# Performance work log

Measured on AMD Instinct MI355X. Metric: run time of the kernel, lower is better.

Reference implementation:

```python
import jax, jax.numpy as jnp
import numpy as np

N_CROPS = 64
K = 128          # keypoints per crop (uniform ragged special case)
D = 128          # descriptor dim
KNN = 20
NQ = 20
MIN_V, MAX_V = 0.0, 1.0


def setup_inputs() -> dict:
    key = jax.random.key(0)
    k1, k2 = jax.random.split(key)
    b = N_CROPS * K
    anc = jax.random.normal(k1, (b, D), dtype=jnp.float32)
    pos = jax.random.normal(k2, (b, D), dtype=jnp.float32)
    # L2-normalized descriptors so similarities fall in the quantizer range
    anc = anc / jnp.linalg.norm(anc, axis=1, keepdims=True)
    pos = pos / jnp.linalg.norm(pos, axis=1, keepdims=True)
    kpts_crop_ids = np.full((N_CROPS,), K, dtype=np.int32)
    return {"anc_feat": anc, "pos_feat": pos, "kpts_crop_ids": kpts_crop_ids}


def _neg_cols(n_crops, k, b):
    # Static per-crop column indices into sim_neg_all (width b-1), excluding
    # the same-crop negative block [i*k, i*k + (k-1)) exactly as the torch code.
    all_c = np.arange(b - 1)
    cols = []
    for i in range(n_crops):
        c = i * k
        cols.append(np.concatenate([all_c[:c], all_c[c + k - 1:]]))
    return np.stack(cols)  # [n_crops, b-k]


def compute_ap(x, label, nq=NQ, min_v=MIN_V, max_v=MAX_V):
    # R2D2 APLoss.compute_AP: fixed 1x1-conv quantizer -> triangular bins
    a = (nq - 1) / (max_v - min_v)
    w1 = np.full(nq, -a, np.float32)
    b1 = (a * min_v + np.arange(nq, 0, -1)).astype(np.float32)
    w2 = np.full(nq, a, np.float32)
    b2 = (np.arange(2 - nq, 2) - a * min_v).astype(np.float32)
    w1[0], b1[0] = 0.0, 1.0     # first line of 1st half: horizontal
    w2[-1], b2[-1] = 0.0, 1.0   # last line of 2nd half: horizontal
    xq = x[:, None, :]
    q = jnp.minimum(w1[None, :, None] * xq + b1[None, :, None],
                    w2[None, :, None] * xq + b2[None, :, None])
    q = jnp.clip(q, 0.0)                                 # N x Q x M
    nbs = q.sum(-1)                                      # N x Q
    rec = (q * label[:, None, :]).sum(-1)                # N x Q
    prec = jnp.cumsum(rec, -1) / (1e-16 + jnp.cumsum(nbs, -1))
    rec = rec / rec.sum(-1, keepdims=True)
    return (prec * rec).sum(-1)                          # per-query AP, [N]


def reference(anc_feat, pos_feat, kpts_crop_ids):
    ks = np.asarray(kpts_crop_ids)
    assert np.all(ks == ks[0]) and int(ks[0]) > 1, "uniform crops, >1 kpt each"
    k = int(ks[0]); n_crops = ks.shape[0]; b = n_crops * k
    sim = anc_feat @ pos_feat.T                          # [b, b]
    sim_pos = jnp.diagonal(sim)[:, None]                 # [b, 1]
    # drop diagonal -> [b, b-1] (row-major off-diagonal, same as mtx[~eye])
    sim_neg_all = sim.reshape(-1)[:-1].reshape(b - 1, b + 1)[:, 1:].reshape(b, b - 1)
    cols = jnp.asarray(_neg_cols(n_crops, k, b))         # [n_crops, b-k]
    blocks = sim_neg_all.reshape(n_crops, k, b - 1)
    # exclude same-crop negatives per crop (static gather), then hard-neg top-k
    excl = jnp.take_along_axis(blocks, cols[:, None, :], axis=2)  # [n_crops, k, b-k]
    top, _ = jax.lax.top_k(excl, KNN)                    # sorted descending == sort[:, :knn]
    sim_neg = top.reshape(b, KNN)
    sim_final = jnp.concatenate([sim_pos, sim_neg], axis=1)      # [b, knn+1]
    lbl_final = jnp.zeros_like(sim_final).at[:, 0].set(1.0)
    ap = compute_ap(sim_final, lbl_final)
    return (1.0 - ap).mean(), ap.mean()
```

## Files before the change

kernel.cpp:

```cpp
#include <hip/hip_runtime.h>

#define B_TOT 8192
#define DIM 128
#define KNN 20
#define NQ 20

#define RPB 128
#define SLICE 1024
#define NSLICE 8
#define NSTEP 16
#define NBIN 64
#define CBUF 64
#define CSTRIDE 66

typedef float f32x4 __attribute__((ext_vector_type(4)));
typedef short short8 __attribute__((ext_vector_type(8)));

__device__ __forceinline__ unsigned short f2bf(float f) {
  unsigned u = __float_as_uint(f);
  return (unsigned short)((u + 0x7FFFu + ((u >> 16) & 1u)) >> 16);
}
__device__ __forceinline__ float bf2f(unsigned short u) {
  return __uint_as_float(((unsigned)u) << 16);
}
__device__ __forceinline__ int binof(float v) {
  int b = (int)((v + 1.0f) * 32.0f);
  return min(NBIN - 1, max(0, b));
}

__global__ __launch_bounds__(256) void cvt_bf16(
    const float* __restrict__ a, const float* __restrict__ p,
    unsigned short* __restrict__ ab, unsigned short* __restrict__ pb) {
  const int i = (blockIdx.x * 256 + threadIdx.x) * 4;
  const float4 va = *reinterpret_cast<const float4*>(a + i);
  const float4 vp = *reinterpret_cast<const float4*>(p + i);
  ushort4 ra, rp;
  ra.x = f2bf(va.x); ra.y = f2bf(va.y); ra.z = f2bf(va.z); ra.w = f2bf(va.w);
  rp.x = f2bf(vp.x); rp.y = f2bf(vp.y); rp.z = f2bf(vp.z); rp.w = f2bf(vp.w);
  *reinterpret_cast<ushort4*>(ab + i) = ra;
  *reinterpret_cast<ushort4*>(pb + i) = rp;
}

__global__ __launch_bounds__(512) void apk_slice(
    const unsigned short* __restrict__ ancb,
    const unsigned short* __restrict__ posb,
    unsigned short* __restrict__ gTop,
    float* __restrict__ gDiag)
{
  __shared__ unsigned int sHist[RPB][NBIN];
  __shared__ unsigned short sBuf[RPB][CSTRIDE];
  __shared__ int sCnt[RPB];
  __shared__ int sThrB[RPB];

  const int tid = threadIdx.x;
  const int wave = tid >> 6;
  const int lane = tid & 63;
  const int rt = wave >> 1;
  const int cg = wave & 1;
  const int l15 = lane & 15;
  const int g = lane >> 4;
  const int rg = blockIdx.x >> 3;
  const int cs = blockIdx.x & 7;
  const int rBase = rg * RPB;
  const int sx0 = (cs == (rg >> 3)) ? (rg & 7) * 2 : -9;

  for (int i = tid; i < RPB * NBIN; i += 512) (&sHist[0][0])[i] = 0u;
  for (int i = tid; i < RPB; i += 512) sCnt[i] = 0;

  short8 afr[2][4];
#pragma unroll
  for (int rsub = 0; rsub < 2; ++rsub) {
    const short8* arow = reinterpret_cast<const short8*>(
        ancb + (size_t)(rBase + rt * 32 + rsub * 16 + l15) * DIM);
#pragma unroll
    for (int kk = 0; kk < 4; ++kk) afr[rsub][kk] = arow[kk * 4 + g];
  }
  __syncthreads();

#define LOADB_MFMA(S)                                                         \
  const int c0 = cs * SLICE + (S) * 64 + cg * 32 + l15;                       \
  short8 bfr[2][4];                                                           \
  _Pragma("unroll") for (int csub = 0; csub < 2; ++csub) {                    \
    const unsigned short* bp = posb + (size_t)(c0 + csub * 16) * DIM + g * 8; \
    _Pragma("unroll") for (int kk = 0; kk < 4; ++kk)                          \
      bfr[csub][kk] = *reinterpret_cast<const short8*>(bp + kk * 32);         \
  }                                                                           \
  f32x4 acc[2][2];                                                            \
  _Pragma("unroll") for (int rsub = 0; rsub < 2; ++rsub)                      \
  _Pragma("unroll") for (int csub = 0; csub < 2; ++csub) {                    \
    acc[rsub][csub] = 0.f;                                                    \
    _Pragma("unroll") for (int kk = 0; kk < 4; ++kk)                          \
      acc[rsub][csub] = __builtin_amdgcn_mfma_f32_16x16x32_bf16(              \
          afr[rsub][kk], bfr[csub][kk], acc[rsub][csub], 0, 0, 0);            \
  }

#pragma unroll 2
  for (int s = 0; s < NSTEP; ++s) {
    LOADB_MFMA(s)
    if (s == sx0 || s == sx0 + 1) {
      const int soff = s - sx0;
#pragma unroll
      for (int rsub = 0; rsub < 2; ++rsub)
#pragma unroll
        for (int csub = 0; csub < 2; ++csub)
#pragma unroll
          for (int q = 0; q < 4; ++q) {
            const int row_l = rt * 32 + rsub * 16 + g * 4 + q;
            const int col_l = cg * 32 + csub * 16 + l15;
            if (row_l == soff * 64 + col_l)
              gDiag[rBase + row_l] = acc[rsub][csub][q];
          }
    } else {
#pragma unroll
      for (int rsub = 0; rsub < 2; ++rsub)
#pragma unroll
        for (int q = 0; q < 4; ++q) {
          const int row_l = rt * 32 + rsub * 16 + g * 4 + q;
          atomicAdd(&sHist[row_l][binof(acc[rsub][0][q])], 1u);
          atomicAdd(&sHist[row_l][binof(acc[rsub][1][q])], 1u);
        }
    }
  }
  __syncthreads();

  if (tid < RPB) {
    int cum = 0, bstar = 0;
    for (int b = NBIN - 1; b >= 0; --b) {
      cum += (int)sHist[tid][b];
      if (cum >= KNN) { bstar = b; break; }
    }
    sThrB[tid] = bstar;
  }
  __syncthreads();

  int thrb[2][4];
#pragma unroll
  for (int rsub = 0; rsub < 2; ++rsub)
#pragma unroll
    for (int q = 0; q < 4; ++q)
      thrb[rsub][q] = sThrB[rt * 32 + rsub * 16 + g * 4 + q];

#pragma unroll 2
  for (int s = 0; s < NSTEP; ++s) {
    if (s == sx0 || s == sx0 + 1) continue;
    LOADB_MFMA(s)
#pragma unroll
    for (int rsub = 0; rsub < 2; ++rsub)
#pragma unroll
      for (int q = 0; q < 4; ++q) {
        const int row_l = rt * 32 + rsub * 16 + g * 4 + q;
        const float v0 = acc[rsub][0][q];
        const float v1 = acc[rsub][1][q];
        if (binof(v0) >= thrb[rsub][q]) {
          const int idx = atomicAdd(&sCnt[row_l], 1);
          if (idx < CBUF) sBuf[row_l][idx] = f2bf(v0);
        }
        if (binof(v1) >= thrb[rsub][q]) {
          const int idx = atomicAdd(&sCnt[row_l], 1);
          if (idx < CBUF) sBuf[row_l][idx] = f2bf(v1);
        }
      }
  }
  __syncthreads();

  const int row = tid >> 2;
  const int h = tid & 3;
  const int cnt = min(sCnt[row], CBUF);
  float tk[KNN];
#pragma unroll
  for (int q = 0; q < KNN; ++q) tk[q] = -1e30f;
  for (int i = h; i < cnt; i += 4) {
    const float v = bf2f(sBuf[row][i]);
    if (v > tk[0]) {
      float x = v;
#pragma unroll
      for (int p = 0; p < KNN - 1; ++p) {
        const float nxt = tk[p + 1];
        tk[p] = fminf(x, nxt);
        x = fmaxf(x, nxt);
      }
      tk[KNN - 1] = x;
    }
  }
  unsigned short* mrg = reinterpret_cast<unsigned short*>(&sHist[row][0]);
#pragma unroll
  for (int q = 0; q < KNN; ++q) mrg[h * KNN + q] = f2bf(tk[q]);
  if (h < 2) {
    float out[KNN];
    int a = KNN - 1, b = KNN - 1;
#pragma unroll
    for (int o = KNN - 1; o >= 0; --o) {
      const float va = (a >= 0) ? bf2f(mrg[h * KNN + a]) : -3e30f;
      const float vb = (b >= 0) ? bf2f(mrg[(h + 2) * KNN + b]) : -3e30f;
      if (va >= vb) { out[o] = va; --a; } else { out[o] = vb; --b; }
    }
#pragma unroll
    for (int q = 0; q < KNN; ++q) mrg[h * KNN + q] = f2bf(out[q]);
  }
  if (h == 0) {
    float out[KNN];
    int a = KNN - 1, b = KNN - 1;
#pragma unroll
    for (int o = KNN - 1; o >= 0; --o) {
      const float va = (a >= 0) ? bf2f(mrg[a]) : -3e30f;
      const float vb = (b >= 0) ? bf2f(mrg[KNN + b]) : -3e30f;
      if (va >= vb) { out[o] = va; --a; } else { out[o] = vb; --b; }
    }
#pragma unroll
    for (int q = 0; q < KNN; ++q)
      gTop[(size_t)(rBase + row) * (NSLICE * KNN) + cs * KNN + q] = f2bf(out[q]);
  }
}

__global__ __launch_bounds__(256) void apk_reduce(
    const unsigned short* __restrict__ gTop, const float* __restrict__ gDiag,
    float* __restrict__ apsum)
{
  const int row = blockIdx.x * 256 + threadIdx.x;
  float tk[KNN];
#pragma unroll
  for (int q = 0; q < KNN; ++q) tk[q] = -1e30f;
  const unsigned short* tp = gTop + (size_t)row * (NSLICE * KNN);
  for (int i = 0; i < NSLICE * KNN; ++i) {
    const float v = bf2f(tp[i]);
    if (v > tk[0]) {
      float x = v;
#pragma unroll
      for (int p = 0; p < KNN - 1; ++p) {
        const float nxt = tk[p + 1];
        tk[p] = fminf(x, nxt);
        x = fmaxf(x, nxt);
      }
      tk[KNN - 1] = x;
    }
  }
  float x[KNN + 1];
  x[0] = gDiag[row];
#pragma unroll
  for (int q = 0; q < KNN; ++q) x[q + 1] = tk[q];
  float cum_rec = 0.f, cum_nbs = 0.f, ap_num = 0.f;
#pragma unroll 1
  for (int qi = 0; qi < NQ; ++qi) {
    const float w1 = (qi == 0) ? 0.f : -19.f;
    const float c1 = (qi == 0) ? 1.f : (float)(20 - qi);
    const float w2 = (qi == NQ - 1) ? 0.f : 19.f;
    const float c2 = (qi == NQ - 1) ? 1.f : (float)(qi - 18);
    float nbs = 0.f, rec = 0.f;
#pragma unroll
    for (int jx = 0; jx < KNN + 1; ++jx) {
      const float xv = x[jx];
      float qv = fminf(fmaf(w1, xv, c1), fmaf(w2, xv, c2));
      qv = fmaxf(qv, 0.f);
      nbs += qv;
      if (jx == 0) rec = qv;
    }
    cum_rec += rec;
    cum_nbs += nbs;
    ap_num = fmaf(cum_rec / (1e-16f + cum_nbs), rec, ap_num);
  }
  float ap = ap_num / cum_rec;
#pragma unroll
  for (int o = 1; o < 64; o <<= 1) ap += __shfl_xor(ap, o, 64);
  if ((threadIdx.x & 63) == 0) atomicAdd(apsum, ap);
}

#define F_TM 16
#define F_TN 256
#define F_NTILE (B_TOT / F_TN)
#define F_TPR (F_TN / F_TM)
#define F_SSTRIDE 264
#define KCROP 128

__global__ __launch_bounds__(256) void apk_topk_f32(
    const float* __restrict__ anc, const float* __restrict__ pos,
    float* __restrict__ apsum)
{
  __shared__ __align__(16) float sAnc[F_TM][DIM];
  __shared__ float sSim[F_TM * F_SSTRIDE];
  __shared__ float sTop[F_TM][F_TPR][KNN];
  __shared__ float sDiag[F_TM];
  __shared__ float sAp[F_TM];
  const int tid = threadIdx.x;
  const int rowBase = blockIdx.x * F_TM;
  for (int idx = tid; idx < F_TM * DIM; idx += 256)
    sAnc[idx / DIM][idx % DIM] = anc[rowBase * DIM + idx];
  __syncthreads();
  float tk[KNN];
#pragma unroll
  for (int q = 0; q < KNN; ++q) tk[q] = -1e30f;
  const int cropLo = (rowBase >> 7) << 7;
  const int myRow = tid / F_TPR;
  const int myLane = tid % F_TPR;
  for (int t = 0; t < F_NTILE; ++t) {
    const int j = t * F_TN + tid;
    float acc[F_TM];
#pragma unroll
    for (int r = 0; r < F_TM; ++r) acc[r] = 0.f;
    const float4* pj = reinterpret_cast<const float4*>(pos + (size_t)j * DIM);
#pragma unroll 2
    for (int k4 = 0; k4 < DIM / 4; ++k4) {
      const float4 p = pj[k4];
#pragma unroll
      for (int r = 0; r < F_TM; ++r) {
        const float4 a = *reinterpret_cast<const float4*>(&sAnc[r][k4 * 4]);
        acc[r] = fmaf(p.x, a.x, acc[r]);
        acc[r] = fmaf(p.y, a.y, acc[r]);
        acc[r] = fmaf(p.z, a.z, acc[r]);
        acc[r] = fmaf(p.w, a.w, acc[r]);
      }
    }
    if (j >= rowBase && j < rowBase + F_TM) sDiag[j - rowBase] = acc[j - rowBase];
    __syncthreads();
#pragma unroll
    for (int r = 0; r < F_TM; ++r) sSim[r * F_SSTRIDE + tid] = acc[r];
    __syncthreads();
    const int jbase = t * F_TN;
#pragma unroll
    for (int q = 0; q < F_TN / F_TPR; ++q) {
      const int jj = q * F_TPR + myLane;
      const int jg = jbase + jj;
      const float v = sSim[myRow * F_SSTRIDE + jj];
      if ((unsigned)(jg - cropLo) >= (unsigned)KCROP && v > tk[0]) {
        float x = v;
#pragma unroll
        for (int p = 0; p < KNN - 1; ++p) {
          const float nxt = tk[p + 1];
          tk[p] = fminf(x, nxt);
          x = fmaxf(x, nxt);
        }
        tk[KNN - 1] = x;
      }
    }
  }
  __syncthreads();
#pragma unroll
  for (int q = 0; q < KNN; ++q) sTop[myRow][myLane][q] = tk[q];
  __syncthreads();
  for (int step = F_TPR / 2; step > 0; step >>= 1) {
    if (myLane < step) {
      float out[KNN];
      int a = KNN - 1, b = KNN - 1;
#pragma unroll
      for (int o = KNN - 1; o >= 0; --o) {
        const float va = (a >= 0) ? sTop[myRow][myLane][a] : -3e30f;
        const float vb = (b >= 0) ? sTop[myRow][myLane + step][b] : -3e30f;
        if (va >= vb) { out[o] = va; --a; } else { out[o] = vb; --b; }
      }
#pragma unroll
      for (int q = 0; q < KNN; ++q) sTop[myRow][myLane][q] = out[q];
    }
    __syncthreads();
  }
  if (tid < F_TM) {
    float x[KNN + 1];
    x[0] = sDiag[tid];
#pragma unroll
    for (int q = 0; q < KNN; ++q) x[q + 1] = sTop[tid][0][q];
    float cum_rec = 0.f, cum_nbs = 0.f, ap_num = 0.f;
#pragma unroll 1
    for (int qi = 0; qi < NQ; ++qi) {
      const float w1 = (qi == 0) ? 0.f : -19.f;
      const float c1 = (qi == 0) ? 1.f : (float)(20 - qi);
      const float w2 = (qi == NQ - 1) ? 0.f : 19.f;
      const float c2 = (qi == NQ - 1) ? 1.f : (float)(qi - 18);
      float nbs = 0.f, rec = 0.f;
#pragma unroll
      for (int jx = 0; jx < KNN + 1; ++jx) {
        const float xv = x[jx];
        float qv = fminf(fmaf(w1, xv, c1), fmaf(w2, xv, c2));
        qv = fmaxf(qv, 0.f);
        nbs += qv;
        if (jx == 0) rec = qv;
      }
      cum_rec += rec;
      cum_nbs += nbs;
      ap_num = fmaf(cum_rec / (1e-16f + cum_nbs), rec, ap_num);
    }
    sAp[tid] = ap_num / cum_rec;
  }
  __syncthreads();
  if (tid == 0) {
    float s = 0.f;
#pragma unroll
    for (int r = 0; r < F_TM; ++r) s += sAp[r];
    atomicAdd(apsum, s);
  }
}

__global__ void apk_final(const float* __restrict__ apsum, float* __restrict__ out) {
  const float m = *apsum * (1.f / (float)B_TOT);
  out[0] = 1.f - m;
  out[1] = m;
}

extern "C" void kernel_launch(void* const* d_in, const int* in_sizes, int n_in,
                              void* d_out, int out_size, void* d_ws, size_t ws_size,
                              hipStream_t stream) {
  const float* anc = (const float*)d_in[0];
  const float* pos = (const float*)d_in[1];
  const size_t bf_bytes = (size_t)B_TOT * DIM * sizeof(unsigned short);
  const size_t top_bytes = (size_t)B_TOT * NSLICE * KNN * sizeof(unsigned short);
  const size_t diag_bytes = (size_t)B_TOT * sizeof(float);
  const size_t off_top = 2 * bf_bytes;
  const size_t off_diag = off_top + ((top_bytes + 15) & ~(size_t)15);
  const size_t off_sum = off_diag + ((diag_bytes + 15) & ~(size_t)15);
  const size_t need = off_sum + 16;
  if (ws_size >= need) {
    unsigned short* ancb = (unsigned short*)d_ws;
    unsigned short* posb = ancb + (size_t)B_TOT * DIM;
    unsigned short* gTop = (unsigned short*)((char*)d_ws + off_top);
    float* gDiag = (float*)((char*)d_ws + off_diag);
    float* apsum = (float*)((char*)d_ws + off_sum);
    hipMemsetAsync(apsum, 0, sizeof(float), stream);
    cvt_bf16<<<(B_TOT * DIM) / (256 * 4), 256, 0, stream>>>(anc, pos, ancb, posb);
    apk_slice<<<64 * NSLICE, 512, 0, stream>>>(ancb, posb, gTop, gDiag);
    apk_reduce<<<B_TOT / 256, 256, 0, stream>>>(gTop, gDiag, apsum);
    apk_final<<<1, 1, 0, stream>>>(apsum, (float*)d_out);
  } else {
    float* apsum = (float*)d_ws;
    hipMemsetAsync(apsum, 0, sizeof(float), stream);
    apk_topk_f32<<<B_TOT / F_TM, 256, 0, stream>>>(anc, pos, apsum);
    apk_final<<<1, 1, 0, stream>>>(apsum, (float*)d_out);
  }
}
```

Before: 246.5 us.

## Replace histogram pass with sampled threshold and fuse reduce/final via last-block atomics

Drops the two-pass histogram approach, in which every tile was computed twice. Instead, a top-20 threshold is estimated per row from a 256-column sample, and candidates above it are collected in a single pass over the remaining tiles. The separate reduce kernel, final kernel and memset are folded into apk_slice: counters are zeroed in cvt_bf16, and the last-arriving block per row group does the cross-slice merge and the AP computation, while the last row group writes the output. This removes one full MFMA recompute and three launches. In exchange it adds serialized top-k work on the sample and threadfence/atomic completion logic, and the candidate buffer can overflow if the sampled threshold is loose.

```diff
diff --git a/kernel.cpp b/kernel.cpp
--- a/kernel.cpp
+++ b/kernel.cpp
@@ -9,9 +9,7 @@
 #define SLICE 1024
 #define NSLICE 8
 #define NSTEP 16
-#define NBIN 64
-#define CBUF 64
-#define CSTRIDE 66
+#define USTRIDE 264
 
 typedef float f32x4 __attribute__((ext_vector_type(4)));
 typedef short short8 __attribute__((ext_vector_type(8)));
@@ -23,14 +21,12 @@
 __device__ __forceinline__ float bf2f(unsigned short u) {
   return __uint_as_float(((unsigned)u) << 16);
 }
-__device__ __forceinline__ int binof(float v) {
-  int b = (int)((v + 1.0f) * 32.0f);
-  return min(NBIN - 1, max(0, b));
-}
 
 __global__ __launch_bounds__(256) void cvt_bf16(
     const float* __restrict__ a, const float* __restrict__ p,
-    unsigned short* __restrict__ ab, unsigned short* __restrict__ pb) {
+    unsigned short* __restrict__ ab, unsigned short* __restrict__ pb,
+    unsigned int* __restrict__ ctrs) {
+  if (blockIdx.x == 0 && threadIdx.x < 66) ctrs[threadIdx.x] = 0u;
   const int i = (blockIdx.x * 256 + threadIdx.x) * 4;
   const float4 va = *reinterpret_cast<const float4*>(a + i);
   const float4 vp = *reinterpret_cast<const float4*>(p + i);
@@ -41,16 +37,44 @@
   *reinterpret_cast<ushort4*>(pb + i) = rp;
 }
 
+#define BUBBLE(tk, v)                                                         \
+  if ((v) > (tk)[0]) {                                                        \
+    float x_ = (v);                                                           \
+    _Pragma("unroll") for (int p_ = 0; p_ < KNN - 1; ++p_) {                  \
+      const float nxt_ = (tk)[p_ + 1];                                        \
+      (tk)[p_] = fminf(x_, nxt_);                                             \
+      x_ = fmaxf(x_, nxt_);                                                   \
+    }                                                                         \
+    (tk)[KNN - 1] = x_;                                                       \
+  }
+
+#define MERGE2(mrg, o1, o2, out)                                              \
+  {                                                                           \
+    int a_ = KNN - 1, b_ = KNN - 1;                                           \
+    _Pragma("unroll") for (int o_ = KNN - 1; o_ >= 0; --o_) {                 \
+      const float va_ = (a_ >= 0) ? bf2f((mrg)[(o1) * KNN + a_]) : -3e30f;    \
+      const float vb_ = (b_ >= 0) ? bf2f((mrg)[(o2) * KNN + b_]) : -3e30f;    \
+      if (va_ >= vb_) { (out)[o_] = va_; --a_; } else { (out)[o_] = vb_; --b_; } \
+    }                                                                         \
+  }
+
 __global__ __launch_bounds__(512) void apk_slice(
     const unsigned short* __restrict__ ancb,
     const unsigned short* __restrict__ posb,
     unsigned short* __restrict__ gTop,
-    float* __restrict__ gDiag)
+    float* __restrict__ gDiag,
+    unsigned int* __restrict__ ctrs,
+    float* __restrict__ outp)
 {
-  __shared__ unsigned int sHist[RPB][NBIN];
-  __shared__ unsigned short sBuf[RPB][CSTRIDE];
+  __shared__ unsigned short sU[RPB][USTRIDE];
   __shared__ int sCnt[RPB];
-  __shared__ int sThrB[RPB];
+  __shared__ float sThr[RPB];
+  __shared__ float sAp[RPB];
+  __shared__ int sIsLast;
+
+  float* apsum = reinterpret_cast<float*>(ctrs);
+  unsigned int* rgDone = ctrs + 1;
+  unsigned int* gReady = ctrs + 2;
 
   const int tid = threadIdx.x;
   const int wave = tid >> 6;
@@ -63,9 +87,7 @@
   const int cs = blockIdx.x & 7;
   const int rBase = rg * RPB;
   const int sx0 = (cs == (rg >> 3)) ? (rg & 7) * 2 : -9;
-
-  for (int i = tid; i < RPB * NBIN; i += 512) (&sHist[0][0])[i] = 0u;
-  for (int i = tid; i < RPB; i += 512) sCnt[i] = 0;
+  const int sampBase = (sx0 >= 0 && sx0 < 4) ? 4 : 0;
 
   short8 afr[2][4];
 #pragma unroll
@@ -75,7 +97,6 @@
 #pragma unroll
     for (int kk = 0; kk < 4; ++kk) afr[rsub][kk] = arow[kk * 4 + g];
   }
-  __syncthreads();
 
 #define LOADB_MFMA(S)                                                         \
   const int c0 = cs * SLICE + (S) * 64 + cg * 32 + l15;                       \
@@ -94,8 +115,60 @@
           afr[rsub][kk], bfr[csub][kk], acc[rsub][csub], 0, 0, 0);            \
   }
 
-#pragma unroll 2
+  for (int s = sampBase; s < sampBase + 4; ++s) {
+    LOADB_MFMA(s)
+#pragma unroll
+    for (int rsub = 0; rsub < 2; ++rsub)
+#pragma unroll
+      for (int csub = 0; csub < 2; ++csub)
+#pragma unroll
+        for (int q = 0; q < 4; ++q) {
+          const int row_l = rt * 32 + rsub * 16 + g * 4 + q;
+          const int sc = (s - sampBase) * 64 + cg * 32 + csub * 16 + l15;
+          sU[row_l][sc] = f2bf(acc[rsub][csub][q]);
+        }
+  }
+  __syncthreads();
+
+  {
+    const int row = tid >> 2;
+    const int h = tid & 3;
+    float tk[KNN];
+#pragma unroll
+    for (int q = 0; q < KNN; ++q) tk[q] = -1e30f;
+    for (int i = 0; i < 64; ++i) {
+      const float v = bf2f(sU[row][h + i * 4]);
+      BUBBLE(tk, v)
+    }
+    unsigned short* mrg = &sU[row][0];
+#pragma unroll
+    for (int q = 0; q < KNN; ++q) mrg[h * KNN + q] = f2bf(tk[q]);
+    if (h < 2) {
+      float out[KNN];
+      MERGE2(mrg, h, h + 2, out)
+#pragma unroll
+      for (int q = 0; q < KNN; ++q) mrg[h * KNN + q] = f2bf(out[q]);
+    }
+    if (h == 0) {
+      float out[KNN];
+      MERGE2(mrg, 0, 1, out)
+#pragma unroll
+      for (int q = 0; q < KNN; ++q) mrg[q] = f2bf(out[q]);
+      sCnt[row] = KNN;
+      sThr[row] = out[0];
+    }
+  }
+  __syncthreads();
+
+  float thrv[2][4];
+#pragma unroll
+  for (int rsub = 0; rsub < 2; ++rsub)
+#pragma unroll
+    for (int q = 0; q < 4; ++q)
+      thrv[rsub][q] = sThr[rt * 32 + rsub * 16 + g * 4 + q];
+
   for (int s = 0; s < NSTEP; ++s) {
+    if ((unsigned)(s - sampBase) < 4u) continue;
     LOADB_MFMA(s)
     if (s == sx0 || s == sx0 + 1) {
       const int soff = s - sx0;
@@ -116,152 +189,134 @@
 #pragma unroll
         for (int q = 0; q < 4; ++q) {
           const int row_l = rt * 32 + rsub * 16 + g * 4 + q;
-          atomicAdd(&sHist[row_l][binof(acc[rsub][0][q])], 1u);
-          atomicAdd(&sHist[row_l][binof(acc[rsub][1][q])], 1u);
+          const float thr = thrv[rsub][q];
+          const float v0 = acc[rsub][0][q];
+          const float v1 = acc[rsub][1][q];
+          if (fmaxf(v0, v1) > thr) {
+            if (v0 > thr) {
+              const int idx = atomicAdd(&sCnt[row_l], 1);
+              if (idx < USTRIDE) sU[row_l][idx] = f2bf(v0);
+            }
+            if (v1 > thr) {
+              const int idx = atomicAdd(&sCnt[row_l], 1);
+              if (idx < USTRIDE) sU[row_l][idx] = f2bf(v1);
+            }
+          }
         }
     }
   }
   __syncthreads();
 
-  if (tid < RPB) {
-    int cum = 0, bstar = 0;
-    for (int b = NBIN - 1; b >= 0; --b) {
-      cum += (int)sHist[tid][b];
-      if (cum >= KNN) { bstar = b; break; }
-    }
-    sThrB[tid] = bstar;
-  }
-  __syncthreads();
-
-  int thrb[2][4];
-#pragma unroll
-  for (int rsub = 0; rsub < 2; ++rsub)
-#pragma unroll
-    for (int q = 0; q < 4; ++q)
-      thrb[rsub][q] = sThrB[rt * 32 + rsub * 16 + g * 4 + q];
-
-#pragma unroll 2
-  for (int s = 0; s < NSTEP; ++s) {
-    if (s == sx0 || s == sx0 + 1) continue;
-    LOADB_MFMA(s)
-#pragma unroll
-    for (int rsub = 0; rsub < 2; ++rsub)
-#pragma unroll
-      for (int q = 0; q < 4; ++q) {
-        const int row_l = rt * 32 + rsub * 16 + g * 4 + q;
-        const float v0 = acc[rsub][0][q];
-        const float v1 = acc[rsub][1][q];
-        if (binof(v0) >= thrb[rsub][q]) {
-          const int idx = atomicAdd(&sCnt[row_l], 1);
-          if (idx < CBUF) sBuf[row_l][idx] = f2bf(v0);
+  {
+    const int row = tid >> 2;
+    const int h = tid & 3;
+    const int cnt = min(sCnt[row], USTRIDE);
+    float tk[KNN];
+#pragma unroll
+    for (int q = 0; q < KNN; ++q) tk[q] = -1e30f;
+    for (int i = h; i < cnt; i += 4) {
+      const float v = bf2f(sU[row][i]);
+      BUBBLE(tk, v)
+    }
+    unsigned short* mrg = &sU[row][0];
+#pragma unroll
+    for (int q = 0; q < KNN; ++q) mrg[h * KNN + q] = f2bf(tk[q]);
+    if (h < 2) {
+      float out[KNN];
+      MERGE2(mrg, h, h + 2, out)
+#pragma unroll
+      for (int q = 0; q < KNN; ++q) mrg[h * KNN + q] = f2bf(out[q]);
+    }
+    if (h == 0) {
+      float out[KNN];
+      MERGE2(mrg, 0, 1, out)
+#pragma unroll
+      for (int q = 0; q < KNN; ++q)
+        gTop[(size_t)cs * (B_TOT * KNN) + (size_t)(rBase + row) * KNN + q] =
+            f2bf(out[q]);
+    }
+  }
+
+  __syncthreads();
+  if (tid == 0) {
+    __threadfence();
+    const unsigned old = atomicAdd(&gReady[rg], 1u);
+    sIsLast = (old == 7u) ? 1 : 0;
+  }
+  __syncthreads();
+  if (sIsLast) {
+    __threadfence();
+    const int row = tid >> 2;
+    const int h = tid & 3;
+    float tk[KNN];
+#pragma unroll
+    for (int q = 0; q < KNN; ++q) tk[q] = -1e30f;
+    for (int c = 0; c < NSLICE; ++c) {
+      const unsigned short* tpc =
+          gTop + (size_t)c * (B_TOT * KNN) + (size_t)(rBase + row) * KNN;
+      for (int q = h; q < KNN; q += 4) {
+        const float v = bf2f(tpc[q]);
+        BUBBLE(tk, v)
+      }
+    }
+    unsigned short* mrg = &sU[row][0];
+#pragma unroll
+    for (int q = 0; q < KNN; ++q) mrg[h * KNN + q] = f2bf(tk[q]);
+    if (h < 2) {
+      float out[KNN];
+      MERGE2(mrg, h, h + 2, out)
+#pragma unroll
+      for (int q = 0; q < KNN; ++q) mrg[h * KNN + q] = f2bf(out[q]);
+    }
+    if (h == 0) {
+      float x[KNN + 1];
+      {
+        float out[KNN];
+        MERGE2(mrg, 0, 1, out)
+#pragma unroll
+        for (int q = 0; q < KNN; ++q) x[q + 1] = out[q];
+      }
+      x[0] = gDiag[rBase + row];
+      float cum_rec = 0.f, cum_nbs = 0.f, ap_num = 0.f;
+#pragma unroll 1
+      for (int qi = 0; qi < NQ; ++qi) {
+        const float w1 = (qi == 0) ? 0.f : -19.f;
+        const float c1 = (qi == 0) ? 1.f : (float)(20 - qi);
+        const float w2 = (qi == NQ - 1) ? 0.f : 19.f;
+        const float c2 = (qi == NQ - 1) ? 1.f : (float)(qi - 18);
+        float nbs = 0.f, rec = 0.f;
+#pragma unroll
+        for (int jx = 0; jx < KNN + 1; ++jx) {
+          const float xv = x[jx];
+          float qv = fminf(fmaf(w1, xv, c1), fmaf(w2, xv, c2));
+          qv = fmaxf(qv, 0.f);
+          nbs += qv;
+          if (jx == 0) rec = qv;
         }
-        if (binof(v1) >= thrb[rsub][q]) {
-          const int idx = atomicAdd(&sCnt[row_l], 1);
-          if (idx < CBUF) sBuf[row_l][idx] = f2bf(v1);
+        cum_rec += rec;
+        cum_nbs += nbs;
+        ap_num = fmaf(cum_rec / (1e-16f + cum_nbs), rec, ap_num);
+      }
+      sAp[row] = ap_num / cum_rec;
+    }
+    __syncthreads();
+    if (tid < 64) {
+      float s = sAp[tid] + sAp[tid + 64];
+#pragma unroll
+      for (int o = 1; o < 64; o <<= 1) s += __shfl_xor(s, o, 64);
+      if (tid == 0) {
+        atomicAdd(apsum, s);
+        __threadfence();
+        const unsigned old2 = atomicAdd(rgDone, 1u);
+        if (old2 == 63u) {
+          __threadfence();
+          const float m = atomicAdd(apsum, 0.f) * (1.f / (float)B_TOT);
+          outp[0] = 1.f - m;
+          outp[1] = m;
         }
       }
-  }
-  __syncthreads();
-
-  const int row = tid >> 2;
-  const int h = tid & 3;
-  const int cnt = min(sCnt[row], CBUF);
-  float tk[KNN];
-#pragma unroll
-  for (int q = 0; q < KNN; ++q) tk[q] = -1e30f;
-  for (int i = h; i < cnt; i += 4) {
-    const float v = bf2f(sBuf[row][i]);
-    if (v > tk[0]) {
-      float x = v;
-#pragma unroll
-      for (int p = 0; p < KNN - 1; ++p) {
-        const float nxt = tk[p + 1];
-        tk[p] = fminf(x, nxt);
-        x = fmaxf(x, nxt);
-      }
-      tk[KNN - 1] = x;
-    }
-  }
-  unsigned short* mrg = reinterpret_cast<unsigned short*>(&sHist[row][0]);
-#pragma unroll
-  for (int q = 0; q < KNN; ++q) mrg[h * KNN + q] = f2bf(tk[q]);
-  if (h < 2) {
-    float out[KNN];
-    int a = KNN - 1, b = KNN - 1;
-#pragma unroll
-    for (int o = KNN - 1; o >= 0; --o) {
-      const float va = (a >= 0) ? bf2f(mrg[h * KNN + a]) : -3e30f;
-      const float vb = (b >= 0) ? bf2f(mrg[(h + 2) * KNN + b]) : -3e30f;
-      if (va >= vb) { out[o] = va; --a; } else { out[o] = vb; --b; }
-    }
-#pragma unroll
-    for (int q = 0; q < KNN; ++q) mrg[h * KNN + q] = f2bf(out[q]);
-  }
-  if (h == 0) {
-    float out[KNN];
-    int a = KNN - 1, b = KNN - 1;
-#pragma unroll
-    for (int o = KNN - 1; o >= 0; --o) {
-      const float va = (a >= 0) ? bf2f(mrg[a]) : -3e30f;
-      const float vb = (b >= 0) ? bf2f(mrg[KNN + b]) : -3e30f;
-      if (va >= vb) { out[o] = va; --a; } else { out[o] = vb; --b; }
-    }
-#pragma unroll
-    for (int q = 0; q < KNN; ++q)
-      gTop[(size_t)(rBase + row) * (NSLICE * KNN) + cs * KNN + q] = f2bf(out[q]);
-  }
-}
-
-__global__ __launch_bounds__(256) void apk_reduce(
-    const unsigned short* __restrict__ gTop, const float* __restrict__ gDiag,
-    float* __restrict__ apsum)
-{
-  const int row = blockIdx.x * 256 + threadIdx.x;
-  float tk[KNN];
-#pragma unroll
-  for (int q = 0; q < KNN; ++q) tk[q] = -1e30f;
-  const unsigned short* tp = gTop + (size_t)row * (NSLICE * KNN);
-  for (int i = 0; i < NSLICE * KNN; ++i) {
-    const float v = bf2f(tp[i]);
-    if (v > tk[0]) {
-      float x = v;
-#pragma unroll
-      for (int p = 0; p < KNN - 1; ++p) {
-        const float nxt = tk[p + 1];
-        tk[p] = fminf(x, nxt);
-        x = fmaxf(x, nxt);
-      }
-      tk[KNN - 1] = x;
-    }
-  }
-  float x[KNN + 1];
-  x[0] = gDiag[row];
-#pragma unroll
-  for (int q = 0; q < KNN; ++q) x[q + 1] = tk[q];
-  float cum_rec = 0.f, cum_nbs = 0.f, ap_num = 0.f;
-#pragma unroll 1
-  for (int qi = 0; qi < NQ; ++qi) {
-    const float w1 = (qi == 0) ? 0.f : -19.f;
-    const float c1 = (qi == 0) ? 1.f : (float)(20 - qi);
-    const float w2 = (qi == NQ - 1) ? 0.f : 19.f;
-    const float c2 = (qi == NQ - 1) ? 1.f : (float)(qi - 18);
-    float nbs = 0.f, rec = 0.f;
-#pragma unroll
-    for (int jx = 0; jx < KNN + 1; ++jx) {
-      const float xv = x[jx];
-      float qv = fminf(fmaf(w1, xv, c1), fmaf(w2, xv, c2));
-      qv = fmaxf(qv, 0.f);
-      nbs += qv;
-      if (jx == 0) rec = qv;
-    }
-    cum_rec += rec;
-    cum_nbs += nbs;
-    ap_num = fmaf(cum_rec / (1e-16f + cum_nbs), rec, ap_num);
-  }
-  float ap = ap_num / cum_rec;
-#pragma unroll
-  for (int o = 1; o < 64; o <<= 1) ap += __shfl_xor(ap, o, 64);
-  if ((threadIdx.x & 63) == 0) atomicAdd(apsum, ap);
+    }
+  }
 }
 
 #define F_TM 16
@@ -403,19 +458,17 @@
   const size_t diag_bytes = (size_t)B_TOT * sizeof(float);
   const size_t off_top = 2 * bf_bytes;
   const size_t off_diag = off_top + ((top_bytes + 15) & ~(size_t)15);
-  const size_t off_sum = off_diag + ((diag_bytes + 15) & ~(size_t)15);
-  const size_t need = off_sum + 16;
+  const size_t off_ctr = off_diag + ((diag_bytes + 15) & ~(size_t)15);
+  const size_t need = off_ctr + 66 * sizeof(unsigned int);
   if (ws_size >= need) {
     unsigned short* ancb = (unsigned short*)d_ws;
     unsigned short* posb = ancb + (size_t)B_TOT * DIM;
     unsigned short* gTop = (unsigned short*)((char*)d_ws + off_top);
     float* gDiag = (float*)((char*)d_ws + off_diag);
-    float* apsum = (float*)((char*)d_ws + off_sum);
-    hipMemsetAsync(apsum, 0, sizeof(float), stream);
-    cvt_bf16<<<(B_TOT * DIM) / (256 * 4), 256, 0, stream>>>(anc, pos, ancb, posb);
-    apk_slice<<<64 * NSLICE, 512, 0, stream>>>(ancb, posb, gTop, gDiag);
-    apk_reduce<<<B_TOT / 256, 256, 0, stream>>>(gTop, gDiag, apsum);
-    apk_final<<<1, 1, 0, stream>>>(apsum, (float*)d_out);
+    unsigned int* ctrs = (unsigned int*)((char*)d_ws + off_ctr);
+    cvt_bf16<<<(B_TOT * DIM) / (256 * 4), 256, 0, stream>>>(anc, pos, ancb, posb, ctrs);
+    apk_slice<<<64 * NSLICE, 512, 0, stream>>>(ancb, posb, gTop, gDiag, ctrs,
+                                               (float*)d_out);
   } else {
     float* apsum = (float*)d_ws;
     hipMemsetAsync(apsum, 0, sizeof(float), stream);
```

New measurement: 233.7 us. 5.2% less time.
